# Kernel optimization log

Measured on AMD Instinct MI355X. Metric: run time of the kernel, lower is better.

## Reference

```python
import jax, jax.numpy as jnp
import numpy as np

B, H, W, C = 16, 64, 64, 512
NH, HD = 16, 32
WH = WW = 8
SHIFT = 4
N = WH * WW
NWIN = (H // WH) * (W // WW)
EPS = 1e-6


def _rel_coords_table():
    rh = np.arange(-(WH - 1), WH, dtype=np.float32)
    rw = np.arange(-(WW - 1), WW, dtype=np.float32)
    t = np.expand_dims(np.transpose(np.stack(np.meshgrid(rh, rw)), (1, 2, 0)), 0)
    t[:, :, :, 0] /= WH - 1
    t[:, :, :, 1] /= WW - 1
    t *= 8
    t = np.sign(t) * np.log2(np.abs(t) + 1.0) / np.log2(8)
    return jnp.asarray(t, jnp.float32)  # (1, 2*WW-1, 2*WH-1, 2)


def _rel_pos_index():
    gx, gy = np.meshgrid(np.arange(WH), np.arange(WW))
    coords = np.stack([gy, gx]).reshape(2, -1)
    rel = (coords[:, :, None] - coords[:, None, :]).transpose(1, 2, 0)
    rel[:, :, 0] += WH - 1
    rel[:, :, 1] += WW - 1
    rel[:, :, 0] *= 2 * WW - 1
    return jnp.asarray(rel.sum(-1).reshape(-1), jnp.int32)  # (N*N,)


def _attn_mask():
    img = np.zeros((H, W), np.float32)
    cnt = 0
    for hs in (slice(0, -WH), slice(-WH, -SHIFT), slice(-SHIFT, None)):
        for ws in (slice(0, -WW), slice(-WW, -SHIFT), slice(-SHIFT, None)):
            img[hs, ws] = cnt
            cnt += 1
    mw = img.reshape(H // WH, WH, W // WW, WW).transpose(0, 2, 1, 3).reshape(-1, N)
    am = mw[:, None, :] - mw[:, :, None]
    return jnp.asarray(np.where(am == 0, 0.0, -100.0), jnp.float32)  # (nW, N, N)


REL_TABLE = _rel_coords_table()
REL_IDX = _rel_pos_index()
ATTN_MASK = _attn_mask()


def _ln(x, g, b):
    m = jnp.mean(x, -1, keepdims=True)
    v = jnp.var(x, -1, keepdims=True)
    return (x - m) * jax.lax.rsqrt(v + EPS) * g + b


def _forward(x, q_w, q_b, k_w, v_w, v_b, proj_w, proj_b, tau,
             cpb_w1, cpb_b1, cpb_w2, cpb_b2,
             norm1_g, norm1_b, norm2_g, norm2_b,
             mlp_w1, mlp_b1, mlp_w2, mlp_b2):
    shortcut = x
    xs = x.reshape(B, H, W, C)
    xs = jnp.roll(xs, shift=(-SHIFT, -SHIFT), axis=(1, 2))  # cyclic shift
    # window partition -> (B*nW, N, C)
    xw = xs.reshape(B, H // WH, WH, W // WW, WW, C).transpose(0, 1, 3, 2, 4, 5).reshape(-1, N, C)
    Bw = B * NWIN
    q = (xw @ q_w + q_b).reshape(Bw, N, NH, HD).transpose(0, 2, 1, 3)
    k = (xw @ k_w).reshape(Bw, N, NH, HD).transpose(0, 2, 1, 3)
    v = (xw @ v_w + v_b).reshape(Bw, N, NH, HD).transpose(0, 2, 1, 3)
    # cosine attention
    qn = jnp.linalg.norm(q, axis=-1)[..., :, None]
    kn = jnp.linalg.norm(k, axis=-1)[..., None, :]
    denom = jnp.maximum(qn * kn, 1e-6)
    attn = jnp.einsum('bhnd,bhmd->bhnm', q, k) / denom
    logit_scale = jnp.maximum(tau + jnp.log(10.0), 0.01)  # (1, NH, 1, 1)
    attn = attn * logit_scale
    # continuous relative position bias MLP
    tbl = jax.nn.relu(REL_TABLE @ cpb_w1 + cpb_b1) @ cpb_w2 + cpb_b2
    tbl = tbl.reshape(-1, NH)
    bias = tbl[REL_IDX].reshape(N, N, NH).transpose(2, 0, 1)
    bias = 16.0 * jax.nn.sigmoid(bias)
    attn = attn + bias[None]
    # shifted-window mask
    attn = attn.reshape(B, NWIN, NH, N, N) + ATTN_MASK[None, :, None]
    attn = jax.nn.softmax(attn.reshape(Bw, NH, N, N), axis=-1)
    out = jnp.einsum('bhnm,bhmd->bhnd', attn, v).transpose(0, 2, 1, 3).reshape(Bw, N, C)
    out = out @ proj_w + proj_b
    # window reverse + reverse shift
    out = out.reshape(B, H // WH, W // WW, WH, WW, C).transpose(0, 1, 3, 2, 4, 5).reshape(B, H, W, C)
    out = jnp.roll(out, shift=(SHIFT, SHIFT), axis=(1, 2)).reshape(B, H * W, C)
    # Swin-V2 post-norm residuals
    x = shortcut + _ln(out, norm1_g, norm1_b)
    h = jax.nn.gelu(x @ mlp_w1 + mlp_b1) @ mlp_w2 + mlp_b2
    x = x + _ln(h, norm2_g, norm2_b)
    return x


def setup_inputs() -> dict:
    key = jax.random.key(0)
    ks = jax.random.split(key, 10)
    s = 0.02
    return {
        'x': jax.random.normal(ks[0], (B, H * W, C), jnp.float32),
        'q_w': jax.random.normal(ks[1], (C, C), jnp.float32) * s,
        'q_b': jnp.zeros((C,), jnp.float32),
        'k_w': jax.random.normal(ks[2], (C, C), jnp.float32) * s,
        'v_w': jax.random.normal(ks[3], (C, C), jnp.float32) * s,
        'v_b': jnp.zeros((C,), jnp.float32),
        'proj_w': jax.random.normal(ks[4], (C, C), jnp.float32) * s,
        'proj_b': jnp.zeros((C,), jnp.float32),
        'tau': jax.random.normal(ks[5], (1, NH, 1, 1), jnp.float32) * s,
        'cpb_w1': jax.random.normal(ks[6], (2, 512), jnp.float32) * s,
        'cpb_b1': jnp.zeros((512,), jnp.float32),
        'cpb_w2': jax.random.normal(ks[7], (512, NH), jnp.float32) * s,
        'cpb_b2': jnp.zeros((NH,), jnp.float32),
        'norm1_g': jnp.ones((C,), jnp.float32),
        'norm1_b': jnp.zeros((C,), jnp.float32),
        'norm2_g': jnp.ones((C,), jnp.float32),
        'norm2_b': jnp.zeros((C,), jnp.float32),
        'mlp_w1': jax.random.normal(ks[8], (C, 4 * C), jnp.float32) * s,
        'mlp_b1': jnp.zeros((4 * C,), jnp.float32),
        'mlp_w2': jax.random.normal(ks[9], (4 * C, C), jnp.float32) * s,
        'mlp_b2': jnp.zeros((C,), jnp.float32),
    }


def reference(x, q_w, q_b, k_w, v_w, v_b, proj_w, proj_b, tau,
              cpb_w1, cpb_b1, cpb_w2, cpb_b2,
              norm1_g, norm1_b, norm2_g, norm2_b,
              mlp_w1, mlp_b1, mlp_w2, mlp_b2):
    return _forward(x, q_w, q_b, k_w, v_w, v_b, proj_w, proj_b, tau,
                    cpb_w1, cpb_b1, cpb_w2, cpb_b2,
                    norm1_g, norm1_b, norm2_g, norm2_b,
                    mlp_w1, mlp_b1, mlp_w2, mlp_b2)
```

## Files before the change

kernel.cpp:

```cpp
#include <hip/hip_runtime.h>
#include <cstdint>
#include <cstddef>

typedef __bf16 bf16x8 __attribute__((ext_vector_type(8)));
typedef float  f32x4  __attribute__((ext_vector_type(4)));

__device__ __forceinline__ float bf2f(unsigned short u) {
  union { unsigned int u; float f; } v; v.u = ((unsigned int)u) << 16; return v.f;
}
__device__ __forceinline__ unsigned short f2bf(float f) {
  union { float f; unsigned int u; } v; v.f = f;
  return (unsigned short)((v.u + 0x7fffu + ((v.u >> 16) & 1u)) >> 16);
}
__device__ __forceinline__ void g2lds16(const void* g, void* l) {
  __builtin_amdgcn_global_load_lds((__attribute__((address_space(1))) void*)g,
                                   (__attribute__((address_space(3))) void*)l,
                                   16, 0, 0);
}

template<int EPI>
__global__ __launch_bounds__(512, 2) void gemm256(
    const unsigned short* __restrict__ A, const unsigned short* __restrict__ BT,
    const float* __restrict__ bias, unsigned short* __restrict__ C,
    int M, int N, int K)
{
  __shared__ __align__(16) unsigned short lds[2][2][2][128 * 64];
  const int tid = threadIdx.x;
  const int wave = tid >> 6, lane = tid & 63;
  const int lm = lane & 15, quad = lane >> 4;
  const int wm2 = wave >> 2, wn4 = wave & 3;
  const int ex = (lm & 7) << 3;

  const int nbx = (int)gridDim.x;
  const int nwg = nbx * (int)gridDim.y;
  const int flat = (int)blockIdx.y * nbx + (int)blockIdx.x;
  const int cpx = nwg >> 3;
  const int wg = (flat & 7) * cpx + (flat >> 3);
  const int bm = wg / nbx, bn = wg % nbx;

  const int NT = K >> 6;

  const int sl8 = lane >> 3;
  const int scol = ((lane & 7) ^ sl8) << 3;
  const int r0 = wave * 8 + sl8;
  const unsigned short* Abase = A + (size_t)(bm * 256 + r0) * K + scol;
  const unsigned short* Bbase = BT + (size_t)(bn * 256 + (r0 >> 5) * 64 + (r0 & 31)) * K + scol;

  auto stageA = [&](int bf, int sh, int koff) {
    const unsigned short* s = Abase + (size_t)(sh * 64) * K + koff;
    g2lds16(s,                   &lds[bf][0][sh][wave * 512]);
    g2lds16(s + (size_t)128 * K, &lds[bf][0][sh][4096 + wave * 512]);
  };
  auto stageB = [&](int bf, int sh, int koff) {
    const unsigned short* s = Bbase + (size_t)(sh * 32) * K + koff;
    g2lds16(s,                   &lds[bf][1][sh][wave * 512]);
    g2lds16(s + (size_t)128 * K, &lds[bf][1][sh][4096 + wave * 512]);
  };

  f32x4 acc[8][4];
#pragma unroll
  for (int i = 0; i < 8; i++)
#pragma unroll
    for (int j = 0; j < 4; j++) acc[i][j] = {0.f, 0.f, 0.f, 0.f};
  bf16x8 a[4][2], b0[2][2], b1[2][2];

  stageA(0, 0, 0); stageB(0, 0, 0); stageB(0, 1, 0); stageA(0, 1, 0);
  {
    const int k1 = (NT > 1 ? 64 : 0);
    stageA(1, 0, k1); stageB(1, 0, k1);
  }
  asm volatile("s_waitcnt vmcnt(4)" ::: "memory");
  __builtin_amdgcn_s_barrier();

  for (int t = 0; t < NT; ++t) {
    const int b = t & 1;
    const int kn1 = (t + 1 < NT ? t + 1 : NT - 1) << 6;
    const int kn2 = (t + 2 < NT ? t + 2 : NT - 1) << 6;

#pragma unroll
    for (int mi = 0; mi < 4; mi++)
#pragma unroll
      for (int ks = 0; ks < 2; ks++)
        a[mi][ks] = *(const bf16x8*)&lds[b][0][0][(wm2 * 64 + mi * 16 + lm) * 64 + ((ks * 32 + quad * 8) ^ ex)];
#pragma unroll
    for (int ni = 0; ni < 2; ni++)
#pragma unroll
      for (int ks = 0; ks < 2; ks++)
        b0[ni][ks] = *(const bf16x8*)&lds[b][1][0][(wn4 * 32 + ni * 16 + lm) * 64 + ((ks * 32 + quad * 8) ^ ex)];
    stageB(b ^ 1, 1, kn1);
    __builtin_amdgcn_s_barrier();
    __builtin_amdgcn_s_setprio(1);
#pragma unroll
    for (int mi = 0; mi < 4; mi++)
#pragma unroll
      for (int ni = 0; ni < 2; ni++)
#pragma unroll
        for (int ks = 0; ks < 2; ks++)
          acc[mi][ni] = __builtin_amdgcn_mfma_f32_16x16x32_bf16(a[mi][ks], b0[ni][ks], acc[mi][ni], 0, 0, 0);
    __builtin_amdgcn_s_setprio(0);
    asm volatile("s_waitcnt vmcnt(8)" ::: "memory");
    __builtin_amdgcn_s_barrier();

#pragma unroll
    for (int ni = 0; ni < 2; ni++)
#pragma unroll
      for (int ks = 0; ks < 2; ks++)
        b1[ni][ks] = *(const bf16x8*)&lds[b][1][1][(wn4 * 32 + ni * 16 + lm) * 64 + ((ks * 32 + quad * 8) ^ ex)];
    stageA(b ^ 1, 1, kn1);
    __builtin_amdgcn_s_barrier();
    __builtin_amdgcn_s_setprio(1);
#pragma unroll
    for (int mi = 0; mi < 4; mi++)
#pragma unroll
      for (int ni = 0; ni < 2; ni++)
#pragma unroll
        for (int ks = 0; ks < 2; ks++)
          acc[mi][2 + ni] = __builtin_amdgcn_mfma_f32_16x16x32_bf16(a[mi][ks], b1[ni][ks], acc[mi][2 + ni], 0, 0, 0);
    __builtin_amdgcn_s_setprio(0);
    asm volatile("s_waitcnt vmcnt(8)" ::: "memory");
    __builtin_amdgcn_s_barrier();

#pragma unroll
    for (int mi = 0; mi < 4; mi++)
#pragma unroll
      for (int ks = 0; ks < 2; ks++)
        a[mi][ks] = *(const bf16x8*)&lds[b][0][1][(wm2 * 64 + mi * 16 + lm) * 64 + ((ks * 32 + quad * 8) ^ ex)];
    stageA(b, 0, kn2);
    __builtin_amdgcn_s_barrier();
    __builtin_amdgcn_s_setprio(1);
#pragma unroll
    for (int mi = 0; mi < 4; mi++)
#pragma unroll
      for (int ni = 0; ni < 2; ni++)
#pragma unroll
        for (int ks = 0; ks < 2; ks++)
          acc[4 + mi][ni] = __builtin_amdgcn_mfma_f32_16x16x32_bf16(a[mi][ks], b0[ni][ks], acc[4 + mi][ni], 0, 0, 0);
    __builtin_amdgcn_s_setprio(0);
    asm volatile("s_waitcnt vmcnt(8)" ::: "memory");
    __builtin_amdgcn_s_barrier();

    stageB(b, 0, kn2);
    __builtin_amdgcn_s_barrier();
    __builtin_amdgcn_s_setprio(1);
#pragma unroll
    for (int mi = 0; mi < 4; mi++)
#pragma unroll
      for (int ni = 0; ni < 2; ni++)
#pragma unroll
        for (int ks = 0; ks < 2; ks++)
          acc[4 + mi][2 + ni] = __builtin_amdgcn_mfma_f32_16x16x32_bf16(a[mi][ks], b1[ni][ks], acc[4 + mi][2 + ni], 0, 0, 0);
    __builtin_amdgcn_s_setprio(0);
    asm volatile("s_waitcnt vmcnt(8)" ::: "memory");
    __builtin_amdgcn_s_barrier();
  }

  float bv[4];
#pragma unroll
  for (int jn = 0; jn < 4; jn++)
    bv[jn] = bias ? bias[bn * 256 + wn4 * 64 + jn * 16 + lm] : 0.f;
  const int rb = bm * 256 + wm2 * 128 + quad * 4;
  const int cb = bn * 256 + wn4 * 64 + lm;
#pragma unroll
  for (int im = 0; im < 8; im++)
#pragma unroll
    for (int jn = 0; jn < 4; jn++)
#pragma unroll
      for (int r = 0; r < 4; r++) {
        float v = acc[im][jn][r] + bv[jn];
        if (EPI == 1) {
          float xx = v;
          float u = 1.5957691216057308f * (xx + 0.044715f * xx * xx * xx);
          v = xx / (1.f + __expf(-u));
        }
        C[(size_t)(rb + im * 16 + r) * N + cb + jn * 16] = f2bf(v);
      }
}

__global__ __launch_bounds__(256) void transpose_cast(
    const float* __restrict__ W, unsigned short* __restrict__ WT, int K, int N)
{
  __shared__ float t[32][33];
  int bx = blockIdx.x, by = blockIdx.y;
  int tx = threadIdx.x & 31, ty = threadIdx.x >> 5;
#pragma unroll
  for (int j = 0; j < 4; j++)
    t[ty + j * 8][tx] = W[(size_t)(by * 32 + ty + j * 8) * N + bx * 32 + tx];
  __syncthreads();
#pragma unroll
  for (int j = 0; j < 4; j++)
    WT[(size_t)(bx * 32 + ty + j * 8) * K + by * 32 + tx] = f2bf(t[tx][ty + j * 8]);
}

__global__ __launch_bounds__(256) void shift_part(
    const float* __restrict__ x, unsigned short* __restrict__ xw)
{
  int t = blockIdx.x * 256 + threadIdx.x;
  int row = t >> 7;
  int c = (t & 127) * 4;
  int b = row >> 12, rw_ = row & 4095;
  int wi = rw_ >> 6, p = rw_ & 63;
  int hh = (((wi >> 3) * 8 + (p >> 3)) + 4) & 63;
  int ww = (((wi & 7) * 8 + (p & 7)) + 4) & 63;
  const float4 v = *(const float4*)&x[(((size_t)b * 4096) + hh * 64 + ww) * 512 + c];
  ushort4 o;
  o.x = f2bf(v.x); o.y = f2bf(v.y); o.z = f2bf(v.z); o.w = f2bf(v.w);
  *(ushort4*)&xw[(size_t)row * 512 + c] = o;
}

__global__ __launch_bounds__(256) void qkv_bias_kernel(
    const float* __restrict__ qb, const float* __restrict__ vb, float* __restrict__ o)
{
  int t = blockIdx.x * 256 + threadIdx.x;
  float v = 0.f;
  if (t < 512) v = qb[t];
  else if (t >= 1024) v = vb[t - 1024];
  o[t] = v;
}

__device__ __forceinline__ float relsc(int v) {
  float a = fabsf((float)v) * (8.0f / 7.0f);
  float r = log2f(a + 1.f) * (1.f / 3.f);
  return v < 0 ? -r : r;
}
__global__ __launch_bounds__(512) void cpb_kernel(
    const float* __restrict__ w1, const float* __restrict__ b1,
    const float* __restrict__ w2, const float* __restrict__ b2, float* __restrict__ tbl)
{
  __shared__ float hid[512];
  int p = blockIdx.x;
  int i = p / 15, j = p % 15;
  float fr = relsc(i - 7);
  float fc = relsc(j - 7);
  int t = threadIdx.x;
  float hv = fc * w1[t] + fr * w1[512 + t] + b1[t];
  hid[t] = fmaxf(hv, 0.f);
  __syncthreads();
  if (t < 16) {
    float s = b2[t];
    for (int u = 0; u < 512; u++) s += hid[u] * w2[u * 16 + t];
    tbl[p * 16 + t] = s;
  }
}

__global__ __launch_bounds__(256) void attn_mfma(
    const unsigned short* __restrict__ QKV, const float* __restrict__ tau,
    const float* __restrict__ tbl, unsigned short* __restrict__ Om)
{
  __shared__ __align__(16) unsigned short Qs[64 * 32];
  __shared__ __align__(16) unsigned short Ks[64 * 32];
  __shared__ __align__(16) unsigned short VT[32 * 72];
  __shared__ __align__(16) unsigned short Pb[64 * 72];
  __shared__ float qn[64], kn[64];
  __shared__ float tblh[225];
  __shared__ int scode[64];

  const int tid = threadIdx.x;
  const int wave = tid >> 6, lane = tid & 63;
  const int lm = lane & 15, quad = lane >> 4;
  const int w = blockIdx.x;
  const int wi = w & 63, wr = wi >> 3, wc = wi & 7;
  const size_t wbase = (size_t)w * 64 * 1536;
  const size_t obase = (size_t)w * 64 * 512;

  if (tid < 64) {
    int p = tid;
    int rp = wr * 8 + (p >> 3), cp = wc * 8 + (p & 7);
    scode[p] = (rp < 56 ? 0 : (rp < 60 ? 1 : 2)) * 3 + (cp < 56 ? 0 : (cp < 60 ? 1 : 2));
  }

  const int srow = wave * 16 + (lane >> 2);
  const int scol = (lane & 3) * 8;
  unsigned short* qdst = &Qs[wave * 16 * 32];
  unsigned short* kdst = &Ks[wave * 16 * 32];
  unsigned short* vdst = &Pb[wave * 16 * 32];

  for (int h = 0; h < 16; h++) {
    const size_t gsrc = wbase + (size_t)srow * 1536 + h * 32 + scol;
    g2lds16(QKV + gsrc, qdst);
    g2lds16(QKV + gsrc + 512, kdst);
    g2lds16(QKV + gsrc + 1024, vdst);
    for (int e = tid; e < 225; e += 256) tblh[e] = tbl[e * 16 + h];
    __syncthreads();

    if (tid < 64) {
      float s = 0;
#pragma unroll
      for (int d = 0; d < 32; d++) { float q_ = bf2f(Qs[tid * 32 + d]); s += q_ * q_; }
      qn[tid] = sqrtf(s);
    } else if (tid < 128) {
      int q = tid - 64; float s = 0;
#pragma unroll
      for (int d = 0; d < 32; d++) { float k_ = bf2f(Ks[q * 32 + d]); s += k_ * k_; }
      kn[q] = sqrtf(s);
    }
    for (int e = tid; e < 2048; e += 256) {
      int d = e & 31, q = e >> 5;
      VT[d * 72 + q] = Pb[q * 32 + d];
    }
    __syncthreads();

    bf16x8 af = *reinterpret_cast<const bf16x8*>(&Qs[(wave * 16 + lm) * 32 + quad * 8]);
    f32x4 accS[4];
#pragma unroll
    for (int ni = 0; ni < 4; ni++) {
      bf16x8 bfr = *reinterpret_cast<const bf16x8*>(&Ks[(ni * 16 + lm) * 32 + quad * 8]);
      f32x4 z = {0.f, 0.f, 0.f, 0.f};
      accS[ni] = __builtin_amdgcn_mfma_f32_16x16x32_bf16(af, bfr, z, 0, 0, 0);
    }

    const float scale = fmaxf(tau[h] + 2.302585092994046f, 0.01f);
#pragma unroll
    for (int r = 0; r < 4; r++) {
      int p = wave * 16 + quad * 4 + r;
      float qnp = qn[p];
      int cp = scode[p];
      float sv[4];
#pragma unroll
      for (int ni = 0; ni < 4; ni++) {
        int q = ni * 16 + lm;
        float dot = accS[ni][r];
        float denom = fmaxf(qnp * kn[q], 1e-6f);
        int dr = (p >> 3) - (q >> 3) + 7, dc = (p & 7) - (q & 7) + 7;
        float bv = tblh[dr * 15 + dc];
        bv = 16.f / (1.f + __expf(-bv));
        float mask = (cp == scode[q]) ? 0.f : -100.f;
        sv[ni] = dot / denom * scale + bv + mask;
      }
      float m = fmaxf(fmaxf(sv[0], sv[1]), fmaxf(sv[2], sv[3]));
#pragma unroll
      for (int off = 1; off < 16; off <<= 1) m = fmaxf(m, __shfl_xor(m, off, 64));
      float s = 0;
#pragma unroll
      for (int ni = 0; ni < 4; ni++) { sv[ni] = __expf(sv[ni] - m); s += sv[ni]; }
#pragma unroll
      for (int off = 1; off < 16; off <<= 1) s += __shfl_xor(s, off, 64);
      float inv = 1.f / s;
#pragma unroll
      for (int ni = 0; ni < 4; ni++)
        Pb[p * 72 + ni * 16 + lm] = f2bf(sv[ni] * inv);
    }

    bf16x8 paf[2];
#pragma unroll
    for (int kc = 0; kc < 2; kc++)
      paf[kc] = *reinterpret_cast<const bf16x8*>(&Pb[(wave * 16 + lm) * 72 + kc * 32 + quad * 8]);
    f32x4 accO[2];
#pragma unroll
    for (int n2 = 0; n2 < 2; n2++) {
      f32x4 z = {0.f, 0.f, 0.f, 0.f};
#pragma unroll
      for (int kc = 0; kc < 2; kc++) {
        bf16x8 vb = *reinterpret_cast<const bf16x8*>(&VT[(n2 * 16 + lm) * 72 + kc * 32 + quad * 8]);
        z = __builtin_amdgcn_mfma_f32_16x16x32_bf16(paf[kc], vb, z, 0, 0, 0);
      }
      accO[n2] = z;
    }
#pragma unroll
    for (int n2 = 0; n2 < 2; n2++)
#pragma unroll
      for (int r = 0; r < 4; r++) {
        int p = wave * 16 + quad * 4 + r;
        Om[obase + (size_t)p * 512 + h * 32 + n2 * 16 + lm] = f2bf(accO[n2][r]);
      }
    __syncthreads();
  }
}

__global__ __launch_bounds__(256) void ln1_kernel(
    const float* __restrict__ x, const unsigned short* __restrict__ proj,
    const float* __restrict__ g, const float* __restrict__ b,
    unsigned short* __restrict__ x1b)
{
  __shared__ float r1[4], r2[4], stats[2];
  int tkn = blockIdx.x;
  int bb = tkn >> 12, s = tkn & 4095;
  int h_ = s >> 6, w_ = s & 63;
  int r = (h_ + 60) & 63, cc = (w_ + 60) & 63;
  int wi = (r >> 3) * 8 + (cc >> 3);
  int p = (r & 7) * 8 + (cc & 7);
  size_t src = ((size_t)bb * 4096 + wi * 64 + p) * 512;
  int c = threadIdx.x * 2;
  unsigned int pv = *(const unsigned int*)&proj[src + c];
  float v0 = bf2f((unsigned short)(pv & 0xffff)), v1 = bf2f((unsigned short)(pv >> 16));
  float ls = v0 + v1, lq = v0 * v0 + v1 * v1;
  for (int off = 32; off > 0; off >>= 1) {
    ls += __shfl_down(ls, off, 64);
    lq += __shfl_down(lq, off, 64);
  }
  int wv = threadIdx.x >> 6, ln = threadIdx.x & 63;
  if (ln == 0) { r1[wv] = ls; r2[wv] = lq; }
  __syncthreads();
  if (threadIdx.x == 0) {
    float S1 = r1[0] + r1[1] + r1[2] + r1[3];
    float S2 = r2[0] + r2[1] + r2[2] + r2[3];
    float mean = S1 * (1.f / 512.f);
    float var = S2 * (1.f / 512.f) - mean * mean;
    stats[0] = mean; stats[1] = rsqrtf(var + 1e-6f);
  }
  __syncthreads();
  float mean = stats[0], rstd = stats[1];
  size_t o = (size_t)tkn * 512 + c;
  float2 xv = *(const float2*)&x[o];
  float y0 = (v0 - mean) * rstd * g[c] + b[c] + xv.x;
  float y1 = (v1 - mean) * rstd * g[c + 1] + b[c + 1] + xv.y;
  unsigned int ov = (unsigned int)f2bf(y0) | ((unsigned int)f2bf(y1) << 16);
  *(unsigned int*)&x1b[o] = ov;
}

__global__ __launch_bounds__(256) void ln2_kernel(
    const unsigned short* __restrict__ x1b, const unsigned short* __restrict__ h2,
    const float* __restrict__ g, const float* __restrict__ b,
    float* __restrict__ out)
{
  __shared__ float r1[4], r2[4], stats[2];
  int tkn = blockIdx.x;
  int c = threadIdx.x * 2;
  size_t o = (size_t)tkn * 512 + c;
  unsigned int hv = *(const unsigned int*)&h2[o];
  float v0 = bf2f((unsigned short)(hv & 0xffff)), v1 = bf2f((unsigned short)(hv >> 16));
  float ls = v0 + v1, lq = v0 * v0 + v1 * v1;
  for (int off = 32; off > 0; off >>= 1) {
    ls += __shfl_down(ls, off, 64);
    lq += __shfl_down(lq, off, 64);
  }
  int wv = threadIdx.x >> 6, ln = threadIdx.x & 63;
  if (ln == 0) { r1[wv] = ls; r2[wv] = lq; }
  __syncthreads();
  if (threadIdx.x == 0) {
    float S1 = r1[0] + r1[1] + r1[2] + r1[3];
    float S2 = r2[0] + r2[1] + r2[2] + r2[3];
    float mean = S1 * (1.f / 512.f);
    float var = S2 * (1.f / 512.f) - mean * mean;
    stats[0] = mean; stats[1] = rsqrtf(var + 1e-6f);
  }
  __syncthreads();
  float mean = stats[0], rstd = stats[1];
  unsigned int xv = *(const unsigned int*)&x1b[o];
  float x0 = bf2f((unsigned short)(xv & 0xffff)), x1 = bf2f((unsigned short)(xv >> 16));
  float2 ov;
  ov.x = x0 + (v0 - mean) * rstd * g[c] + b[c];
  ov.y = x1 + (v1 - mean) * rstd * g[c + 1] + b[c + 1];
  *(float2*)&out[o] = ov;
}

extern "C" void kernel_launch(void* const* d_in, const int* in_sizes, int n_in,
                              void* d_out, int out_size, void* d_ws, size_t ws_size,
                              hipStream_t stream) {
  const float* x      = (const float*)d_in[0];
  const float* q_w    = (const float*)d_in[1];
  const float* q_b    = (const float*)d_in[2];
  const float* k_w    = (const float*)d_in[3];
  const float* v_w    = (const float*)d_in[4];
  const float* v_b    = (const float*)d_in[5];
  const float* proj_w = (const float*)d_in[6];
  const float* proj_b = (const float*)d_in[7];
  const float* tau    = (const float*)d_in[8];
  const float* cpb_w1 = (const float*)d_in[9];
  const float* cpb_b1 = (const float*)d_in[10];
  const float* cpb_w2 = (const float*)d_in[11];
  const float* cpb_b2 = (const float*)d_in[12];
  const float* n1g    = (const float*)d_in[13];
  const float* n1b    = (const float*)d_in[14];
  const float* n2g    = (const float*)d_in[15];
  const float* n2b    = (const float*)d_in[16];
  const float* mlp_w1 = (const float*)d_in[17];
  const float* mlp_b1 = (const float*)d_in[18];
  const float* mlp_w2 = (const float*)d_in[19];
  const float* mlp_b2 = (const float*)d_in[20];
  float* out = (float*)d_out;
  char* ws = (char*)d_ws;

  const size_t MB = 1048576;
  unsigned short* xw    = (unsigned short*)(ws + 0 * MB);
  unsigned short* Obuf  = (unsigned short*)(ws + 0 * MB);
  unsigned short* hbuf  = (unsigned short*)(ws + 0 * MB);
  unsigned short* qkv   = (unsigned short*)(ws + 64 * MB);
  unsigned short* projb = (unsigned short*)(ws + 64 * MB);
  unsigned short* x1b   = (unsigned short*)(ws + 128 * MB);
  unsigned short* h2b   = (unsigned short*)(ws + 192 * MB);
  unsigned short* qkvT = (unsigned short*)(ws + 320 * MB);
  unsigned short* pwT  = (unsigned short*)(ws + 320 * MB + 1572864);
  unsigned short* m1T  = (unsigned short*)(ws + 320 * MB + 2097152);
  unsigned short* m2T  = (unsigned short*)(ws + 320 * MB + 4194304);
  float* tbl           = (float*)         (ws + 320 * MB + 6291456);
  float* qkv_b         = (float*)         (ws + 320 * MB + 6307840);

  transpose_cast<<<dim3(16, 16), 256, 0, stream>>>(q_w,    qkvT,          512, 512);
  transpose_cast<<<dim3(16, 16), 256, 0, stream>>>(k_w,    qkvT + 262144, 512, 512);
  transpose_cast<<<dim3(16, 16), 256, 0, stream>>>(v_w,    qkvT + 524288, 512, 512);
  transpose_cast<<<dim3(16, 16), 256, 0, stream>>>(proj_w, pwT, 512, 512);
  transpose_cast<<<dim3(64, 16), 256, 0, stream>>>(mlp_w1, m1T, 512, 2048);
  transpose_cast<<<dim3(16, 64), 256, 0, stream>>>(mlp_w2, m2T, 2048, 512);
  qkv_bias_kernel<<<6, 256, 0, stream>>>(q_b, v_b, qkv_b);
  cpb_kernel<<<225, 512, 0, stream>>>(cpb_w1, cpb_b1, cpb_w2, cpb_b2, tbl);
  shift_part<<<32768, 256, 0, stream>>>(x, xw);
  gemm256<0><<<dim3(6, 256), 512, 0, stream>>>(xw, qkvT, qkv_b, qkv, 65536, 1536, 512);
  attn_mfma<<<1024, 256, 0, stream>>>(qkv, tau, tbl, Obuf);
  gemm256<0><<<dim3(2, 256), 512, 0, stream>>>(Obuf, pwT, proj_b, projb, 65536, 512, 512);
  ln1_kernel<<<65536, 256, 0, stream>>>(x, projb, n1g, n1b, x1b);
  for (int c2 = 0; c2 < 2; c2++) {
    const unsigned short* a = x1b + (size_t)c2 * 32768 * 512;
    unsigned short* h2p = h2b + (size_t)c2 * 32768 * 512;
    gemm256<1><<<dim3(8, 128), 512, 0, stream>>>(a, m1T, mlp_b1, hbuf, 32768, 2048, 512);
    gemm256<0><<<dim3(2, 128), 512, 0, stream>>>(hbuf, m2T, mlp_b2, h2p, 32768, 512, 2048);
  }
  ln2_kernel<<<65536, 256, 0, stream>>>(x1b, h2b, n2g, n2b, out);
}
```

Before: 1.031 ms.

## Split attention heads across blocks, prefetch next head, precompute sigmoid bias

```diff
diff --git a/kernel.cpp b/kernel.cpp
--- a/kernel.cpp
+++ b/kernel.cpp
@@ -4,6 +4,7 @@
 
 typedef __bf16 bf16x8 __attribute__((ext_vector_type(8)));
 typedef float  f32x4  __attribute__((ext_vector_type(4)));
+typedef unsigned short u16x8 __attribute__((ext_vector_type(8)));
 
 __device__ __forceinline__ float bf2f(unsigned short u) {
   union { unsigned int u; float f; } v; v.u = ((unsigned int)u) << 16; return v.f;
@@ -11,6 +12,9 @@
 __device__ __forceinline__ unsigned short f2bf(float f) {
   union { float f; unsigned int u; } v; v.f = f;
   return (unsigned short)((v.u + 0x7fffu + ((v.u >> 16) & 1u)) >> 16);
+}
+__device__ __forceinline__ bf16x8 as_bf(u16x8 u) {
+  union { u16x8 a; bf16x8 b; } v; v.a = u; return v.b;
 }
 __device__ __forceinline__ void g2lds16(const void* g, void* l) {
   __builtin_amdgcn_global_load_lds((__attribute__((address_space(1))) void*)g,
@@ -224,7 +228,7 @@
 }
 __global__ __launch_bounds__(512) void cpb_kernel(
     const float* __restrict__ w1, const float* __restrict__ b1,
-    const float* __restrict__ w2, const float* __restrict__ b2, float* __restrict__ tbl)
+    const float* __restrict__ w2, const float* __restrict__ b2, float* __restrict__ tblT)
 {
   __shared__ float hid[512];
   int p = blockIdx.x;
@@ -238,26 +242,27 @@
   if (t < 16) {
     float s = b2[t];
     for (int u = 0; u < 512; u++) s += hid[u] * w2[u * 16 + t];
-    tbl[p * 16 + t] = s;
+    tblT[t * 225 + p] = 16.f / (1.f + __expf(-s));
   }
 }
 
 __global__ __launch_bounds__(256) void attn_mfma(
     const unsigned short* __restrict__ QKV, const float* __restrict__ tau,
-    const float* __restrict__ tbl, unsigned short* __restrict__ Om)
+    const float* __restrict__ tblT, unsigned short* __restrict__ Om)
 {
   __shared__ __align__(16) unsigned short Qs[64 * 32];
   __shared__ __align__(16) unsigned short Ks[64 * 32];
+  __shared__ __align__(16) unsigned short Vs[64 * 32];
   __shared__ __align__(16) unsigned short VT[32 * 72];
   __shared__ __align__(16) unsigned short Pb[64 * 72];
-  __shared__ float qn[64], kn[64];
-  __shared__ float tblh[225];
+  __shared__ float tblh[2][228];
   __shared__ int scode[64];
 
   const int tid = threadIdx.x;
   const int wave = tid >> 6, lane = tid & 63;
   const int lm = lane & 15, quad = lane >> 4;
-  const int w = blockIdx.x;
+  const int w = blockIdx.x >> 1;
+  const int hbase = (blockIdx.x & 1) * 8;
   const int wi = w & 63, wr = wi >> 3, wc = wi & 7;
   const size_t wbase = (size_t)w * 64 * 1536;
   const size_t obase = (size_t)w * 64 * 512;
@@ -272,72 +277,92 @@
   const int scol = (lane & 3) * 8;
   unsigned short* qdst = &Qs[wave * 16 * 32];
   unsigned short* kdst = &Ks[wave * 16 * 32];
-  unsigned short* vdst = &Pb[wave * 16 * 32];
-
-  for (int h = 0; h < 16; h++) {
-    const size_t gsrc = wbase + (size_t)srow * 1536 + h * 32 + scol;
-    g2lds16(QKV + gsrc, qdst);
-    g2lds16(QKV + gsrc + 512, kdst);
-    g2lds16(QKV + gsrc + 1024, vdst);
-    for (int e = tid; e < 225; e += 256) tblh[e] = tbl[e * 16 + h];
+  unsigned short* vdst = &Vs[wave * 16 * 32];
+  const size_t gs0 = wbase + (size_t)srow * 1536 + scol;
+
+  {
+    const size_t g = gs0 + (size_t)hbase * 32;
+    g2lds16(QKV + g, qdst);
+    g2lds16(QKV + g + 512, kdst);
+    g2lds16(QKV + g + 1024, vdst);
+    for (int e = tid; e < 225; e += 256) tblh[0][e] = tblT[hbase * 225 + e];
+  }
+
+  for (int hh = 0; hh < 8; hh++) {
+    const int h = hbase + hh, cur = hh & 1;
     __syncthreads();
 
-    if (tid < 64) {
-      float s = 0;
-#pragma unroll
-      for (int d = 0; d < 32; d++) { float q_ = bf2f(Qs[tid * 32 + d]); s += q_ * q_; }
-      qn[tid] = sqrtf(s);
-    } else if (tid < 128) {
-      int q = tid - 64; float s = 0;
-#pragma unroll
-      for (int d = 0; d < 32; d++) { float k_ = bf2f(Ks[q * 32 + d]); s += k_ * k_; }
-      kn[q] = sqrtf(s);
+    u16x8 au = *(const u16x8*)&Qs[(wave * 16 + lm) * 32 + quad * 8];
+    float qss = 0.f;
+#pragma unroll
+    for (int j = 0; j < 8; j++) { float f = bf2f(au[j]); qss += f * f; }
+    qss += __shfl_xor(qss, 16, 64);
+    qss += __shfl_xor(qss, 32, 64);
+    const float qnv = sqrtf(qss);
+
+    u16x8 bu[4]; float knv[4];
+#pragma unroll
+    for (int ni = 0; ni < 4; ni++) {
+      bu[ni] = *(const u16x8*)&Ks[(ni * 16 + lm) * 32 + quad * 8];
+      float kss = 0.f;
+#pragma unroll
+      for (int j = 0; j < 8; j++) { float f = bf2f(bu[ni][j]); kss += f * f; }
+      kss += __shfl_xor(kss, 16, 64);
+      kss += __shfl_xor(kss, 32, 64);
+      knv[ni] = sqrtf(kss);
     }
+
+    bf16x8 af = as_bf(au);
+    f32x4 accS[4];
+#pragma unroll
+    for (int ni = 0; ni < 4; ni++) {
+      f32x4 z = {0.f, 0.f, 0.f, 0.f};
+      accS[ni] = __builtin_amdgcn_mfma_f32_16x16x32_bf16(af, as_bf(bu[ni]), z, 0, 0, 0);
+    }
+
     for (int e = tid; e < 2048; e += 256) {
       int d = e & 31, q = e >> 5;
-      VT[d * 72 + q] = Pb[q * 32 + d];
-    }
-    __syncthreads();
-
-    bf16x8 af = *reinterpret_cast<const bf16x8*>(&Qs[(wave * 16 + lm) * 32 + quad * 8]);
-    f32x4 accS[4];
-#pragma unroll
-    for (int ni = 0; ni < 4; ni++) {
-      bf16x8 bfr = *reinterpret_cast<const bf16x8*>(&Ks[(ni * 16 + lm) * 32 + quad * 8]);
-      f32x4 z = {0.f, 0.f, 0.f, 0.f};
-      accS[ni] = __builtin_amdgcn_mfma_f32_16x16x32_bf16(af, bfr, z, 0, 0, 0);
+      VT[d * 72 + q] = Vs[q * 32 + d];
     }
 
     const float scale = fmaxf(tau[h] + 2.302585092994046f, 0.01f);
 #pragma unroll
     for (int r = 0; r < 4; r++) {
       int p = wave * 16 + quad * 4 + r;
-      float qnp = qn[p];
+      float qnp = __shfl(qnv, quad * 4 + r, 64);
       int cp = scode[p];
       float sv[4];
 #pragma unroll
       for (int ni = 0; ni < 4; ni++) {
         int q = ni * 16 + lm;
-        float dot = accS[ni][r];
-        float denom = fmaxf(qnp * kn[q], 1e-6f);
+        float denom = fmaxf(qnp * knv[ni], 1e-6f);
         int dr = (p >> 3) - (q >> 3) + 7, dc = (p & 7) - (q & 7) + 7;
-        float bv = tblh[dr * 15 + dc];
-        bv = 16.f / (1.f + __expf(-bv));
+        float bv = tblh[cur][dr * 15 + dc];
         float mask = (cp == scode[q]) ? 0.f : -100.f;
-        sv[ni] = dot / denom * scale + bv + mask;
+        sv[ni] = accS[ni][r] * scale * __builtin_amdgcn_rcpf(denom) + bv + mask;
       }
       float m = fmaxf(fmaxf(sv[0], sv[1]), fmaxf(sv[2], sv[3]));
 #pragma unroll
       for (int off = 1; off < 16; off <<= 1) m = fmaxf(m, __shfl_xor(m, off, 64));
-      float s = 0;
+      float s = 0.f;
 #pragma unroll
       for (int ni = 0; ni < 4; ni++) { sv[ni] = __expf(sv[ni] - m); s += sv[ni]; }
 #pragma unroll
       for (int off = 1; off < 16; off <<= 1) s += __shfl_xor(s, off, 64);
-      float inv = 1.f / s;
+      float inv = __builtin_amdgcn_rcpf(s);
 #pragma unroll
       for (int ni = 0; ni < 4; ni++)
         Pb[p * 72 + ni * 16 + lm] = f2bf(sv[ni] * inv);
+    }
+
+    __syncthreads();
+
+    if (hh < 7) {
+      const size_t g = gs0 + (size_t)(h + 1) * 32;
+      g2lds16(QKV + g, qdst);
+      g2lds16(QKV + g + 512, kdst);
+      g2lds16(QKV + g + 1024, vdst);
+      for (int e = tid; e < 225; e += 256) tblh[cur ^ 1][e] = tblT[(h + 1) * 225 + e];
     }
 
     bf16x8 paf[2];
@@ -362,7 +387,6 @@
         int p = wave * 16 + quad * 4 + r;
         Om[obase + (size_t)p * 512 + h * 32 + n2 * 16 + lm] = f2bf(accO[n2][r]);
       }
-    __syncthreads();
   }
 }
 
@@ -495,7 +519,7 @@
   cpb_kernel<<<225, 512, 0, stream>>>(cpb_w1, cpb_b1, cpb_w2, cpb_b2, tbl);
   shift_part<<<32768, 256, 0, stream>>>(x, xw);
   gemm256<0><<<dim3(6, 256), 512, 0, stream>>>(xw, qkvT, qkv_b, qkv, 65536, 1536, 512);
-  attn_mfma<<<1024, 256, 0, stream>>>(qkv, tau, tbl, Obuf);
+  attn_mfma<<<2048, 256, 0, stream>>>(qkv, tau, tbl, Obuf);
   gemm256<0><<<dim3(2, 256), 512, 0, stream>>>(Obuf, pwT, proj_b, projb, 65536, 512, 512);
   ln1_kernel<<<65536, 256, 0, stream>>>(x, projb, n1g, n1b, x1b);
   for (int c2 = 0; c2 < 2; c2++) {
```

Result: faster. 1.005 ms (-2.6%).
